# Kernel optimization log

Hardware: AMD Instinct MI355X
Metric: run time of the kernel (lower is better)

Reference implementation:

```python
import jax, jax.numpy as jnp
import numpy as np

NUM_EXPERTS = 8
TOP_K = 2
HIDDEN = 2048
FFN = 4096


def setup_inputs() -> dict:
    key = jax.random.key(0)
    ks = jax.random.split(key, 5)
    s = 0.02
    return {
        "hidden_states": jax.random.normal(ks[0], (2, 2048, HIDDEN), dtype=jnp.float32),
        "w_router": jax.random.normal(ks[1], (HIDDEN, NUM_EXPERTS), dtype=jnp.float32) * s,
        "w1": jax.random.normal(ks[2], (NUM_EXPERTS, FFN, HIDDEN), dtype=jnp.float32) * s,
        "w2": jax.random.normal(ks[3], (NUM_EXPERTS, HIDDEN, FFN), dtype=jnp.float32) * s,
        "w3": jax.random.normal(ks[4], (NUM_EXPERTS, FFN, HIDDEN), dtype=jnp.float32) * s,
    }


def reference(hidden_states, w_router, w1, w2, w3):
    shape = hidden_states.shape
    x = hidden_states.reshape(-1, HIDDEN)  # [T, H]

    # Router: logits -> softmax -> top-k -> renormalize (Mixtral routing)
    logits = x @ w_router                              # [T, E]
    probs = jax.nn.softmax(logits, axis=-1)
    top_w, top_i = jax.lax.top_k(probs, TOP_K)         # [T, K]
    top_w = top_w / jnp.sum(top_w, axis=-1, keepdims=True)
    # Dense combine weights per expert: [T, E]
    combine = jnp.sum(
        jax.nn.one_hot(top_i, NUM_EXPERTS, dtype=x.dtype) * top_w[..., None], axis=1
    )

    # Grouped SwiGLU experts: out = sum_e combine[:, e] * w2_e(silu(w1_e x) * w3_e x)
    out = jnp.zeros_like(x)
    for e in range(NUM_EXPERTS):
        h = jax.nn.silu(x @ w1[e].T) * (x @ w3[e].T)   # [T, F]
        y = h @ w2[e].T                                # [T, H]
        out = out + combine[:, e:e + 1] * y

    return (out.reshape(shape), jnp.zeros((1,), dtype=x.dtype))
```

## Files before the change

kernel.cpp:

```cpp
#include <hip/hip_runtime.h>
#include <hip/hip_bf16.h>
#include <stdint.h>

#define T_TOK 4096
#define HID   2048
#define FFN_D 4096
#define NE    8
#define PADB  256
#define PADMAX 10240

typedef __attribute__((ext_vector_type(8))) short  short8;
typedef __attribute__((ext_vector_type(4))) float  f32x4;
typedef __attribute__((ext_vector_type(4))) unsigned short u16x4;
typedef unsigned short u16;

__device__ __forceinline__ u16 f2bf(float f) {
    unsigned u = __float_as_uint(f);
    u += 0x7FFFu + ((u >> 16) & 1u);
    return (u16)(u >> 16);
}
__device__ __forceinline__ float bf2f(u16 v) {
    return __uint_as_float(((unsigned)v) << 16);
}

#define GLD16(g, l) __builtin_amdgcn_global_load_lds( \
    (const __attribute__((address_space(1))) unsigned int*)(g), \
    (__attribute__((address_space(3))) unsigned int*)(l), 16, 0, 0)

__global__ void k_convert(const float* __restrict__ s, u16* __restrict__ d, long n8) {
    for (long i = (long)blockIdx.x * 256 + threadIdx.x; i < n8; i += (long)gridDim.x * 256) {
        f32x4 a = *((const f32x4*)s + i * 2);
        f32x4 b = *((const f32x4*)s + i * 2 + 1);
        short8 o;
#pragma unroll
        for (int q = 0; q < 4; ++q) { o[q] = (short)f2bf(a[q]); o[q + 4] = (short)f2bf(b[q]); }
        *(short8*)(d + i * 8) = o;
    }
}

__global__ void k_convert2(const float* __restrict__ s0, u16* __restrict__ d0,
                           const float* __restrict__ s1, u16* __restrict__ d1, long n8) {
    for (long i = (long)blockIdx.x * 256 + threadIdx.x; i < 2 * n8; i += (long)gridDim.x * 256) {
        const float* s = (i < n8) ? s0 : s1;
        u16*         d = (i < n8) ? d0 : d1;
        long         j = (i < n8) ? i : (i - n8);
        f32x4 a = *((const f32x4*)s + j * 2);
        f32x4 b = *((const f32x4*)s + j * 2 + 1);
        short8 o;
#pragma unroll
        for (int q = 0; q < 4; ++q) { o[q] = (short)f2bf(a[q]); o[q + 4] = (short)f2bf(b[q]); }
        *(short8*)(d + j * 8) = o;
    }
}

__global__ void k_router(const float* __restrict__ x, const float* __restrict__ wr,
                         u16* __restrict__ xb,
                         int* __restrict__ topk_id, float* __restrict__ topk_w,
                         int* __restrict__ counts) {
    int lane = threadIdx.x & 63;
    int t = blockIdx.x * 4 + (threadIdx.x >> 6);
    const float* xr = x + (size_t)t * HID;
    u16* xbr = xb + (size_t)t * HID;
    float acc[8];
#pragma unroll
    for (int e = 0; e < 8; ++e) acc[e] = 0.f;
    for (int h = lane; h < HID; h += 64) {
        float xv = xr[h];
        xbr[h] = f2bf(xv);
        f32x4 w0 = *(const f32x4*)(wr + h * 8);
        f32x4 w1 = *(const f32x4*)(wr + h * 8 + 4);
#pragma unroll
        for (int q = 0; q < 4; ++q) { acc[q] += xv * w0[q]; acc[4 + q] += xv * w1[q]; }
    }
#pragma unroll
    for (int e = 0; e < 8; ++e) {
        float v = acc[e];
#pragma unroll
        for (int s = 32; s > 0; s >>= 1) v += __shfl_xor(v, s);
        acc[e] = v;
    }
    if (lane == 0) {
        int i0 = 0; float l0 = acc[0];
#pragma unroll
        for (int e = 1; e < 8; ++e) if (acc[e] > l0) { l0 = acc[e]; i0 = e; }
        int i1 = -1; float l1 = -3.4e38f;
#pragma unroll
        for (int e = 0; e < 8; ++e) if (e != i0 && acc[e] > l1) { l1 = acc[e]; i1 = e; }
        float wA = 1.f / (1.f + expf(l1 - l0));
        topk_id[t * 2] = i0;  topk_id[t * 2 + 1] = i1;
        topk_w[t * 2] = wA;   topk_w[t * 2 + 1] = 1.f - wA;
        atomicAdd(&counts[i0], 1);
        atomicAdd(&counts[i1], 1);
    }
}

__global__ void k_scan(const int* __restrict__ counts, int* __restrict__ pad_off,
                       int* __restrict__ perm_tok) {
    __shared__ int sTot;
    if (threadIdx.x == 0) {
        int o = 0;
#pragma unroll
        for (int e = 0; e < 8; ++e) { pad_off[e] = o; o += ((counts[e] + PADB - 1) / PADB) * PADB; }
        pad_off[8] = o; sTot = o;
    }
    __syncthreads();
    int tot = sTot;
    for (int i = threadIdx.x; i < tot; i += 256) perm_tok[i] = 0;
}

__global__ void k_scatter(const int* __restrict__ topk_id, int* __restrict__ cursors,
                          const int* __restrict__ pad_off, int* __restrict__ perm_tok,
                          int* __restrict__ pos_of) {
    int t = blockIdx.x * 256 + threadIdx.x;
    if (t >= T_TOK) return;
#pragma unroll
    for (int k = 0; k < 2; ++k) {
        int e = topk_id[t * 2 + k];
        int p = pad_off[e] + atomicAdd(&cursors[e], 1);
        perm_tok[p] = t;
        pos_of[t * 2 + k] = p;
    }
}

template<int KTOT, int NTOT, int BNt, int KSPLIT, bool DUAL, bool GATHER, bool CONV>
__global__ __launch_bounds__(512, 2) void k_gemm8(
    const u16* __restrict__ A,
    const u16* __restrict__ B0all,
    const u16* __restrict__ B1all,
    u16* __restrict__ C,
    const int* __restrict__ perm_tok,
    const int* __restrict__ pad_off,
    const float* __restrict__ W2c,
    u16* __restrict__ W2d,
    int gemmBlk, int convBlk)
{
    constexpr int BMt   = 256;
    constexpr int WCW   = BNt / 4;
    constexpr int NI    = WCW / 16;
    constexpr int CPX   = (NTOT / BNt) / 8;
    constexpr int KPART = KTOT / KSPLIT;
    constexpr int NK    = KPART / 64;
    constexpr int ATILE = BMt * 64;
    constexpr int BTILE = BNt * 64;
    constexpr int SEGB  = DUAL ? 8 : (BNt == 256 ? 8 : 4);

    const int bid = blockIdx.x;
    const int tid = threadIdx.x;

    if (CONV && bid >= gemmBlk) {
        const long per = (long)NE * FFN_D * HID / 8 / convBlk;
        const long i0 = (long)(bid - gemmBlk) * per;
        for (long i = i0 + tid; i < i0 + per; i += 512) {
            f32x4 a = *((const f32x4*)W2c + i * 2);
            f32x4 b = *((const f32x4*)W2c + i * 2 + 1);
            short8 o;
#pragma unroll
            for (int q = 0; q < 4; ++q) { o[q] = (short)f2bf(a[q]); o[q + 4] = (short)f2bf(b[q]); }
            *(short8*)(W2d + i * 8) = o;
        }
        return;
    }

    const int xcd = bid & 7;
    int idx = bid >> 3;
    const int kh  = idx & (KSPLIT - 1);
    idx /= KSPLIT;
    const int m0  = (idx / CPX) * BMt;
    if (m0 >= pad_off[8]) return;
    const int n0  = (xcd * CPX + (idx % CPX)) * BNt;
    int e = 0;
    while (pad_off[e + 1] <= m0) ++e;

    __shared__ u16 As[2 * ATILE];
    __shared__ u16 Bs0[2 * BTILE];
    __shared__ u16 Bs1[DUAL ? 2 * BTILE : 8];
    __shared__ int tokS[GATHER ? BMt : 8];

    const int w = tid >> 6, l = tid & 63;
    if (GATHER) {
        for (int i = tid; i < BMt; i += 512) tokS[i] = perm_tok[m0 + i];
        __syncthreads();
    }

    const u16* B0 = B0all + (size_t)e * NTOT * KTOT;
    const u16* B1 = DUAL ? (B1all + (size_t)e * NTOT * KTOT) : B0all;
    const int k0e = kh * KPART;

    const int nseg = (w < 4) ? 8 : SEGB;
    const u16* gsrc[8];
    u16* ldst[8];
    int tstep;
    {
        const int c = (l & 7) ^ (l >> 3);
#pragma unroll
        for (int j = 0; j < 8; ++j) {
            const int js = (j < nseg) ? j : (j - 4);
            const int rl = js * 8 + (l >> 3);
            if (w < 4) {
                const int rt = w * 64 + rl;
                const long grow = GATHER ? (long)tokS[rt] : (long)(m0 + rt);
                gsrc[j] = A + grow * KTOT + k0e + c * 8;
                ldst[j] = (u16*)As + (w * 64 + js * 8) * 64;
                tstep = ATILE;
            } else if (DUAL && w >= 6) {
                const int rt = (w - 6) * 64 + rl;
                gsrc[j] = B1 + (size_t)(n0 + rt) * KTOT + k0e + c * 8;
                ldst[j] = (u16*)Bs1 + (rt - rl + js * 8) * 64;
                tstep = BTILE;
            } else {
                const int rt = DUAL ? ((w - 4) * 64 + rl)
                                    : (BNt == 256 ? ((w - 4) * 64 + rl)
                                                  : ((w - 4) * 32 + rl));
                gsrc[j] = B0 + (size_t)(n0 + rt) * KTOT + k0e + c * 8;
                ldst[j] = (u16*)Bs0 + (rt - rl + js * 8) * 64;
                tstep = BTILE;
            }
        }
    }

    const int wr = w >> 2, wc = w & 3;
    const int fr = l & 15, fk = l >> 4, x7 = l & 7;
    const int pc0 = ((fk ^ x7) << 3);
    const int pc1 = pc0 ^ 32;
    const int aB = (wr * 128 + fr) * 64;
    const int bB = (wc * WCW + fr) * 64;

    f32x4 acc0[8][NI], acc1[8][NI];
    const f32x4 fz = {0.f, 0.f, 0.f, 0.f};
#pragma unroll
    for (int mi = 0; mi < 8; ++mi)
#pragma unroll
        for (int ni = 0; ni < NI; ++ni) { acc0[mi][ni] = fz; if (DUAL) acc1[mi][ni] = fz; }

#pragma unroll
    for (int j = 0; j < 8; ++j) if (j < nseg) GLD16(gsrc[j], ldst[j]);
    asm volatile("s_waitcnt vmcnt(0)" ::: "memory");
    __builtin_amdgcn_s_barrier();
    __builtin_amdgcn_sched_barrier(0);

#pragma unroll 1
    for (int t = 0; t < NK; ++t) {
        const int cb = t & 1, nb2 = cb ^ 1;
        const u16* aC  = (const u16*)As  + cb * ATILE;
        const u16* b0C = (const u16*)Bs0 + cb * BTILE;
        const u16* b1C = (const u16*)Bs1 + (DUAL ? cb * BTILE : 0);
        const long kE = (long)(t + 1) * 64;
        const bool hasNext = (t + 1 < NK);

        short8 af[4], b0f[NI], b1f[NI];

        if (hasNext) {
#pragma unroll
            for (int j = 0; j < 4; ++j) if (j < nseg) GLD16(gsrc[j] + kE, ldst[j] + nb2 * tstep);
        }
#pragma unroll
        for (int mi = 0; mi < 4; ++mi) af[mi] = *(const short8*)(aC + aB + mi * 1024 + pc0);
#pragma unroll
        for (int ni = 0; ni < NI; ++ni) {
            b0f[ni] = *(const short8*)(b0C + bB + ni * 1024 + pc0);
            if (DUAL) b1f[ni] = *(const short8*)(b1C + bB + ni * 1024 + pc0);
        }
        __builtin_amdgcn_s_setprio(1);
#pragma unroll
        for (int mi = 0; mi < 4; ++mi)
#pragma unroll
            for (int ni = 0; ni < NI; ++ni) {
                acc0[mi][ni] = __builtin_amdgcn_mfma_f32_16x16x32_bf16(af[mi], b0f[ni], acc0[mi][ni], 0, 0, 0);
                if (DUAL)
                    acc1[mi][ni] = __builtin_amdgcn_mfma_f32_16x16x32_bf16(af[mi], b1f[ni], acc1[mi][ni], 0, 0, 0);
            }
        __builtin_amdgcn_s_setprio(0);

        if (hasNext) {
#pragma unroll
            for (int j = 4; j < 8; ++j) if (j < nseg) GLD16(gsrc[j] + kE, ldst[j] + nb2 * tstep);
        }
#pragma unroll
        for (int mi = 0; mi < 4; ++mi) af[mi] = *(const short8*)(aC + aB + (mi + 4) * 1024 + pc0);
        __builtin_amdgcn_s_setprio(1);
#pragma unroll
        for (int mi = 0; mi < 4; ++mi)
#pragma unroll
            for (int ni = 0; ni < NI; ++ni) {
                acc0[mi + 4][ni] = __builtin_amdgcn_mfma_f32_16x16x32_bf16(af[mi], b0f[ni], acc0[mi + 4][ni], 0, 0, 0);
                if (DUAL)
                    acc1[mi + 4][ni] = __builtin_amdgcn_mfma_f32_16x16x32_bf16(af[mi], b1f[ni], acc1[mi + 4][ni], 0, 0, 0);
            }
        __builtin_amdgcn_s_setprio(0);

#pragma unroll
        for (int mi = 0; mi < 4; ++mi) af[mi] = *(const short8*)(aC + aB + mi * 1024 + pc1);
#pragma unroll
        for (int ni = 0; ni < NI; ++ni) {
            b0f[ni] = *(const short8*)(b0C + bB + ni * 1024 + pc1);
            if (DUAL) b1f[ni] = *(const short8*)(b1C + bB + ni * 1024 + pc1);
        }
        __builtin_amdgcn_s_setprio(1);
#pragma unroll
        for (int mi = 0; mi < 4; ++mi)
#pragma unroll
            for (int ni = 0; ni < NI; ++ni) {
                acc0[mi][ni] = __builtin_amdgcn_mfma_f32_16x16x32_bf16(af[mi], b0f[ni], acc0[mi][ni], 0, 0, 0);
                if (DUAL)
                    acc1[mi][ni] = __builtin_amdgcn_mfma_f32_16x16x32_bf16(af[mi], b1f[ni], acc1[mi][ni], 0, 0, 0);
            }
        __builtin_amdgcn_s_setprio(0);

#pragma unroll
        for (int mi = 0; mi < 4; ++mi) af[mi] = *(const short8*)(aC + aB + (mi + 4) * 1024 + pc1);
        __builtin_amdgcn_s_setprio(1);
#pragma unroll
        for (int mi = 0; mi < 4; ++mi)
#pragma unroll
            for (int ni = 0; ni < NI; ++ni) {
                acc0[mi + 4][ni] = __builtin_amdgcn_mfma_f32_16x16x32_bf16(af[mi], b0f[ni], acc0[mi + 4][ni], 0, 0, 0);
                if (DUAL)
                    acc1[mi + 4][ni] = __builtin_amdgcn_mfma_f32_16x16x32_bf16(af[mi], b1f[ni], acc1[mi + 4][ni], 0, 0, 0);
            }
        __builtin_amdgcn_s_setprio(0);

        asm volatile("s_waitcnt vmcnt(0)" ::: "memory");
        __builtin_amdgcn_s_barrier();
        __builtin_amdgcn_sched_barrier(0);
    }

    u16* Co = C + (KSPLIT > 1 ? (size_t)kh * PADMAX * NTOT : 0);
    const int er = (l >> 4) * 4;
    const int ec = l & 15;
#pragma unroll
    for (int mi = 0; mi < 8; ++mi)
#pragma unroll
        for (int ni = 0; ni < NI; ++ni)
#pragma unroll
            for (int r = 0; r < 4; ++r) {
                size_t prow = (size_t)(m0 + wr * 128 + mi * 16 + er + r);
                int col = n0 + wc * WCW + ni * 16 + ec;
                float v = acc0[mi][ni][r];
                float res;
                if (DUAL) {
                    float g3 = acc1[mi][ni][r];
                    res = v / (1.f + __expf(-v)) * g3;
                } else {
                    res = v;
                }
                Co[prow * NTOT + col] = f2bf(res);
            }
}

__global__ void k_combine2(const u16* __restrict__ y0, const u16* __restrict__ y1,
                           const int* __restrict__ pos_of,
                           const float* __restrict__ topk_w, float* __restrict__ out) {
    int idx = blockIdx.x * 256 + threadIdx.x;
    int t  = idx >> 9;
    int c4 = (idx & 511) << 2;
    int p0 = pos_of[t * 2], p1 = pos_of[t * 2 + 1];
    float w0 = topk_w[t * 2], w1 = topk_w[t * 2 + 1];
    u16x4 a0 = *(const u16x4*)(y0 + (size_t)p0 * HID + c4);
    u16x4 a1 = *(const u16x4*)(y1 + (size_t)p0 * HID + c4);
    u16x4 b0 = *(const u16x4*)(y0 + (size_t)p1 * HID + c4);
    u16x4 b1 = *(const u16x4*)(y1 + (size_t)p1 * HID + c4);
    f32x4 o;
#pragma unroll
    for (int q = 0; q < 4; ++q)
        o[q] = w0 * (bf2f(a0[q]) + bf2f(a1[q])) + w1 * (bf2f(b0[q]) + bf2f(b1[q]));
    *(f32x4*)(out + (size_t)t * HID + c4) = o;
    if (idx == 0) out[(size_t)T_TOK * HID] = 0.f;
}

__global__ void k_init(int* __restrict__ c) {
    if (threadIdx.x < 16) c[threadIdx.x] = 0;
}

extern "C" void kernel_launch(void* const* d_in, const int* in_sizes, int n_in,
                              void* d_out, int out_size, void* d_ws, size_t ws_size,
                              hipStream_t stream) {
    const float* x  = (const float*)d_in[0];
    const float* wr = (const float*)d_in[1];
    const float* w1 = (const float*)d_in[2];
    const float* w2 = (const float*)d_in[3];
    const float* w3 = (const float*)d_in[4];
    float* out = (float*)d_out;
    char* ws = (char*)d_ws;

    const long WN8 = (long)NE * FFN_D * HID / 8;
    const size_t NEED = 503459840ull;

    if (ws_size >= NEED) {
        u16*  xb  = (u16*)(ws);
        u16*  wA  = (u16*)(ws + 16777216);
        u16*  w3b = (u16*)(ws + 150994944);
        u16*  hb  = (u16*)(ws + 285212672);
        u16*  w2b = (u16*)(ws + 369098752);
        u16*  yb  = (u16*)(ws + 150994944);
        int*  perm_tok = (int*)(ws + 503316480);
        int*  pos_of   = (int*)(ws + 503357440);
        int*  topk_id  = (int*)(ws + 503390208);
        float* topk_w  = (float*)(ws + 503422976);
        int*  cnt      = (int*)(ws + 503455744);
        int*  counts   = cnt;
        int*  cursors  = cnt + 8;
        int*  pad_off  = cnt + 16;

        k_init<<<1, 64, 0, stream>>>(cnt);
        k_router<<<1024, 256, 0, stream>>>(x, wr, xb, topk_id, topk_w, counts);
        k_scan<<<1, 256, 0, stream>>>(counts, pad_off, perm_tok);
        k_scatter<<<16, 256, 0, stream>>>(topk_id, cursors, pad_off, perm_tok, pos_of);

        k_convert2<<<8192, 256, 0, stream>>>(w1, wA, w3, w3b, WN8);

        k_gemm8<HID, FFN_D, 128, 1, true, true, true>
            <<<(FFN_D / 128) * 40 + 512, 512, 0, stream>>>(
            xb, wA, w3b, hb, perm_tok, pad_off, w2, w2b, (FFN_D / 128) * 40, 512);

        k_gemm8<FFN_D, HID, 256, 2, false, false, false>
            <<<(HID / 256) * 40 * 2, 512, 0, stream>>>(
            hb, w2b, (const u16*)nullptr, yb, perm_tok, pad_off,
            (const float*)nullptr, (u16*)nullptr, 0, 0);

        k_combine2<<<8192, 256, 0, stream>>>(yb, yb + (size_t)PADMAX * HID,
                                             pos_of, topk_w, out);
    } else {
        u16*  xb  = (u16*)(ws);
        u16*  wA  = (u16*)(ws + 16777216);
        u16*  w3b = (u16*)(ws + 150994944);
        u16*  hb  = (u16*)(ws + 285212672);
        u16*  yb  = (u16*)(ws + 150994944);
        int*  perm_tok = (int*)(ws + 369098752);
        int*  pos_of   = (int*)(ws + 369139712);
        int*  topk_id  = (int*)(ws + 369172480);
        float* topk_w  = (float*)(ws + 369205248);
        int*  cnt      = (int*)(ws + 369238016);
        int*  counts   = cnt;
        int*  cursors  = cnt + 8;
        int*  pad_off  = cnt + 16;

        k_init<<<1, 64, 0, stream>>>(cnt);
        k_router<<<1024, 256, 0, stream>>>(x, wr, xb, topk_id, topk_w, counts);
        k_scan<<<1, 256, 0, stream>>>(counts, pad_off, perm_tok);
        k_scatter<<<16, 256, 0, stream>>>(topk_id, cursors, pad_off, perm_tok, pos_of);

        k_convert2<<<8192, 256, 0, stream>>>(w1, wA, w3, w3b, WN8);

        k_gemm8<HID, FFN_D, 128, 1, true, true, false>
            <<<(FFN_D / 128) * 40, 512, 0, stream>>>(
            xb, wA, w3b, hb, perm_tok, pad_off,
            (const float*)nullptr, (u16*)nullptr, 0, 0);

        k_convert<<<4096, 256, 0, stream>>>(w2, wA, WN8);

        k_gemm8<FFN_D, HID, 256, 2, false, false, false>
            <<<(HID / 256) * 40 * 2, 512, 0, stream>>>(
            hb, wA, (const u16*)nullptr, yb, perm_tok, pad_off,
            (const float*)nullptr, (u16*)nullptr, 0, 0);

        k_combine2<<<8192, 256, 0, stream>>>(yb, yb + (size_t)PADMAX * HID,
                                             pos_of, topk_w, out);
    }
}
```

Baseline: 853.1 us.

## Fuse router with weight conversion and split second GEMM K into four partials

```diff
diff --git a/kernel.cpp b/kernel.cpp
--- a/kernel.cpp
+++ b/kernel.cpp
@@ -53,12 +53,13 @@
     }
 }
 
-__global__ void k_router(const float* __restrict__ x, const float* __restrict__ wr,
-                         u16* __restrict__ xb,
-                         int* __restrict__ topk_id, float* __restrict__ topk_w,
-                         int* __restrict__ counts) {
-    int lane = threadIdx.x & 63;
-    int t = blockIdx.x * 4 + (threadIdx.x >> 6);
+__device__ __forceinline__ void router_body(
+    int blk, int tid,
+    const float* __restrict__ x, const float* __restrict__ wr,
+    u16* __restrict__ xb, int* __restrict__ topk_id,
+    float* __restrict__ topk_w, int* __restrict__ counts) {
+    int lane = tid & 63;
+    int t = blk * 4 + (tid >> 6);
     const float* xr = x + (size_t)t * HID;
     u16* xbr = xb + (size_t)t * HID;
     float acc[8];
@@ -91,6 +92,35 @@
         topk_w[t * 2] = wA;   topk_w[t * 2 + 1] = 1.f - wA;
         atomicAdd(&counts[i0], 1);
         atomicAdd(&counts[i1], 1);
+    }
+}
+
+__global__ void k_router(const float* __restrict__ x, const float* __restrict__ wr,
+                         u16* __restrict__ xb, int* __restrict__ topk_id,
+                         float* __restrict__ topk_w, int* __restrict__ counts) {
+    router_body(blockIdx.x, threadIdx.x, x, wr, xb, topk_id, topk_w, counts);
+}
+
+__global__ void k_pre(const float* __restrict__ x, const float* __restrict__ wr,
+                      u16* __restrict__ xb, int* __restrict__ topk_id,
+                      float* __restrict__ topk_w, int* __restrict__ counts,
+                      const float* __restrict__ w1, u16* __restrict__ w1b,
+                      const float* __restrict__ w3, u16* __restrict__ w3b, long n8) {
+    if (blockIdx.x < 1024) {
+        router_body(blockIdx.x, threadIdx.x, x, wr, xb, topk_id, topk_w, counts);
+        return;
+    }
+    const long nb = (long)(gridDim.x - 1024);
+    for (long i = (long)(blockIdx.x - 1024) * 256 + threadIdx.x; i < 2 * n8; i += nb * 256) {
+        const float* s = (i < n8) ? w1 : w3;
+        u16*         d = (i < n8) ? w1b : w3b;
+        long         j = (i < n8) ? i : (i - n8);
+        f32x4 a = *((const f32x4*)s + j * 2);
+        f32x4 b = *((const f32x4*)s + j * 2 + 1);
+        short8 o;
+#pragma unroll
+        for (int q = 0; q < 4; ++q) { o[q] = (short)f2bf(a[q]); o[q + 4] = (short)f2bf(b[q]); }
+        *(short8*)(d + j * 8) = o;
     }
 }
 
@@ -347,6 +377,26 @@
             }
 }
 
+__global__ void k_combine4(const u16* __restrict__ y, const int* __restrict__ pos_of,
+                           const float* __restrict__ topk_w, float* __restrict__ out) {
+    int idx = blockIdx.x * 256 + threadIdx.x;
+    int t  = idx >> 9;
+    int c4 = (idx & 511) << 2;
+    int p0 = pos_of[t * 2], p1 = pos_of[t * 2 + 1];
+    float w0 = topk_w[t * 2], w1 = topk_w[t * 2 + 1];
+    const size_t PS = (size_t)PADMAX * HID;
+    f32x4 o = {0.f, 0.f, 0.f, 0.f};
+#pragma unroll
+    for (int p = 0; p < 4; ++p) {
+        u16x4 a = *(const u16x4*)(y + p * PS + (size_t)p0 * HID + c4);
+        u16x4 b = *(const u16x4*)(y + p * PS + (size_t)p1 * HID + c4);
+#pragma unroll
+        for (int q = 0; q < 4; ++q) o[q] += w0 * bf2f(a[q]) + w1 * bf2f(b[q]);
+    }
+    *(f32x4*)(out + (size_t)t * HID + c4) = o;
+    if (idx == 0) out[(size_t)T_TOK * HID] = 0.f;
+}
+
 __global__ void k_combine2(const u16* __restrict__ y0, const u16* __restrict__ y1,
                            const int* __restrict__ pos_of,
                            const float* __restrict__ topk_w, float* __restrict__ out) {
@@ -391,7 +441,7 @@
         u16*  w3b = (u16*)(ws + 150994944);
         u16*  hb  = (u16*)(ws + 285212672);
         u16*  w2b = (u16*)(ws + 369098752);
-        u16*  yb  = (u16*)(ws + 150994944);
+        u16*  yb  = (u16*)(ws + 16777216);
         int*  perm_tok = (int*)(ws + 503316480);
         int*  pos_of   = (int*)(ws + 503357440);
         int*  topk_id  = (int*)(ws + 503390208);
@@ -402,23 +452,22 @@
         int*  pad_off  = cnt + 16;
 
         k_init<<<1, 64, 0, stream>>>(cnt);
-        k_router<<<1024, 256, 0, stream>>>(x, wr, xb, topk_id, topk_w, counts);
+
+        k_pre<<<9216, 256, 0, stream>>>(x, wr, xb, topk_id, topk_w, counts,
+                                        w1, wA, w3, w3b, WN8);
         k_scan<<<1, 256, 0, stream>>>(counts, pad_off, perm_tok);
         k_scatter<<<16, 256, 0, stream>>>(topk_id, cursors, pad_off, perm_tok, pos_of);
-
-        k_convert2<<<8192, 256, 0, stream>>>(w1, wA, w3, w3b, WN8);
 
         k_gemm8<HID, FFN_D, 128, 1, true, true, true>
             <<<(FFN_D / 128) * 40 + 512, 512, 0, stream>>>(
             xb, wA, w3b, hb, perm_tok, pad_off, w2, w2b, (FFN_D / 128) * 40, 512);
 
-        k_gemm8<FFN_D, HID, 256, 2, false, false, false>
-            <<<(HID / 256) * 40 * 2, 512, 0, stream>>>(
+        k_gemm8<FFN_D, HID, 256, 4, false, false, false>
+            <<<(HID / 256) * 40 * 4, 512, 0, stream>>>(
             hb, w2b, (const u16*)nullptr, yb, perm_tok, pad_off,
             (const float*)nullptr, (u16*)nullptr, 0, 0);
 
-        k_combine2<<<8192, 256, 0, stream>>>(yb, yb + (size_t)PADMAX * HID,
-                                             pos_of, topk_w, out);
+        k_combine4<<<8192, 256, 0, stream>>>(yb, pos_of, topk_w, out);
     } else {
         u16*  xb  = (u16*)(ws);
         u16*  wA  = (u16*)(ws + 16777216);
```

Result: faster. 826.2 us (median of 4 runs) (-3.2%).
